# Kernel tuning notes

Measured on AMD Instinct MI355X. Metric: run time of the kernel, lower is better.

Reference implementation:

```python
import jax, jax.numpy as jnp
import numpy as np

B, S, D = 2, 2048, 2048
H = 16
Q_LORA, KV_LORA = 1536, 512
D_NOPE, D_ROPE, D_V = 128, 64, 128
QK_D = D_NOPE + D_ROPE  # 192
EPS = 1e-6
ROPE_THETA = 10000.0


def rms_norm(x, w, eps=EPS):
    return x * jax.lax.rsqrt(jnp.mean(x * x, axis=-1, keepdims=True) + eps) * w


def apply_rope(x, cos, sin):
    # x: [b, s, h, d]; cos/sin: [s, d//2]; pairs are interleaved (x0,x1),(x2,x3),...
    xr, xi = x[..., 0::2], x[..., 1::2]
    c = cos[None, :, None, :]
    s = sin[None, :, None, :]
    yr = xr * c - xi * s
    yi = xr * s + xi * c
    return jnp.stack([yr, yi], axis=-1).reshape(x.shape)


def setup_inputs() -> dict:
    key = jax.random.key(0)
    ks = jax.random.split(key, 8)
    sd = 0.02
    pos = jnp.arange(S, dtype=jnp.float32)
    inv_freq = 1.0 / (ROPE_THETA ** (jnp.arange(0, D_ROPE, 2, dtype=jnp.float32) / D_ROPE))
    ang = pos[:, None] * inv_freq[None, :]  # [S, D_ROPE//2]
    mask = jnp.triu(jnp.full((S, S), float('-inf'), dtype=jnp.float32), k=1)
    return {
        'x': jax.random.normal(ks[0], (B, S, D), dtype=jnp.float32),
        'freqs_cos': jnp.cos(ang),
        'freqs_sin': jnp.sin(ang),
        'mask': mask,
        'wq_a': jax.random.normal(ks[1], (Q_LORA, D), dtype=jnp.float32) * sd,
        'q_norm_w': jnp.ones((Q_LORA,), dtype=jnp.float32),
        'wq_b': jax.random.normal(ks[2], (H * QK_D, Q_LORA), dtype=jnp.float32) * sd,
        'wkv_a': jax.random.normal(ks[3], (KV_LORA + D_ROPE, D), dtype=jnp.float32) * sd,
        'kv_norm_w': jnp.ones((KV_LORA,), dtype=jnp.float32),
        'wkv_b': jax.random.normal(ks[4], (H * (D_NOPE + D_V), KV_LORA), dtype=jnp.float32) * sd,
        'wo': jax.random.normal(ks[5], (D, H * D_V), dtype=jnp.float32) * sd,
    }


def reference(x, freqs_cos, freqs_sin, mask, wq_a, q_norm_w, wq_b, wkv_a, kv_norm_w, wkv_b, wo):
    b, s, _ = x.shape
    # query path: down-proj -> RMSNorm -> up-proj
    q = rms_norm(x @ wq_a.T, q_norm_w) @ wq_b.T          # [b, s, H*QK_D]
    q = q.reshape(b, s, H, QK_D)
    q_nope, q_pe = q[..., :D_NOPE], q[..., D_NOPE:]
    q_pe = apply_rope(q_pe, freqs_cos, freqs_sin)
    # kv path: joint down-proj, split latent / rope key
    kv_full = x @ wkv_a.T                                 # [b, s, KV_LORA + D_ROPE]
    kv, k_pe = kv_full[..., :KV_LORA], kv_full[..., KV_LORA:]
    k_pe = apply_rope(k_pe[:, :, None, :], freqs_cos, freqs_sin)  # [b, s, 1, D_ROPE]
    q = jnp.concatenate([q_nope, q_pe], axis=-1)          # [b, s, H, QK_D]
    kv = rms_norm(kv, kv_norm_w) @ wkv_b.T                # [b, s, H*(D_NOPE+D_V)]
    kv = kv.reshape(b, s, H, D_NOPE + D_V)
    k_nope, v = kv[..., :D_NOPE], kv[..., D_NOPE:]
    k = jnp.concatenate([k_nope, jnp.broadcast_to(k_pe, (b, s, H, D_ROPE))], axis=-1)
    scale = QK_D ** -0.5
    scores = jnp.einsum('bshd,bthd->bsht', q, k) * scale + mask[None, :, None, :]
    probs = jax.nn.softmax(scores.astype(jnp.float32), axis=-1).astype(x.dtype)
    out = jnp.einsum('bsht,bthd->bshd', probs, v).reshape(b, s, H * D_V)
    return out @ wo.T
```

## Files before the change

kernel.cpp:

```cpp
#include <hip/hip_runtime.h>
#include <hip/hip_bf16.h>

typedef __bf16 bf16_t;
typedef __bf16 bf16x8 __attribute__((ext_vector_type(8)));
typedef __bf16 bf16x4 __attribute__((ext_vector_type(4)));
typedef __bf16 bf16x2 __attribute__((ext_vector_type(2)));
typedef float  f32x4  __attribute__((ext_vector_type(4)));
typedef float  f32x16 __attribute__((ext_vector_type(16)));

#define NB 2
#define NS 2048
#define ND 2048
#define NH 16
#define QLORA 1536
#define KVLORA 512
#define DNOPE 128
#define DROPE 64
#define DVDIM 128
#define QKD 192

#define QSCALE 0.10411754f

#if __has_builtin(__builtin_amdgcn_exp2f)
#define EXP2F(x) __builtin_amdgcn_exp2f(x)
#else
#define EXP2F(x) __expf((x) * 0.69314718056f)
#endif
#if __has_builtin(__builtin_amdgcn_rcpf)
#define RCPF(x) __builtin_amdgcn_rcpf(x)
#else
#define RCPF(x) (1.0f / (x))
#endif

typedef __attribute__((address_space(3))) void as3_void;
typedef __attribute__((address_space(1))) const void as1_void;
__device__ __forceinline__ void gload16(const void* g, void* l) {
  __builtin_amdgcn_global_load_lds((as1_void*)g, (as3_void*)l, 16, 0, 0);
}

__device__ __forceinline__ int pack2(float a, float b) {
  bf16x2 t = {(bf16_t)a, (bf16_t)b};
  return __builtin_bit_cast(int, t);
}

__global__ __launch_bounds__(256) void k_cvt_all(
    const float* __restrict__ x, const float* __restrict__ wqa,
    const float* __restrict__ wqb, const float* __restrict__ wkva,
    const float* __restrict__ wkvb, const float* __restrict__ wo,
    bf16_t* __restrict__ xb, bf16_t* __restrict__ wqab, bf16_t* __restrict__ wqbb,
    bf16_t* __restrict__ wkvab, bf16_t* __restrict__ wkvbb, bf16_t* __restrict__ wob) {
  const int c0 = 2097152, c1 = 2883584, c2 = 4063232, c3 = 4358144, c4 = 4882432,
            c5 = 5931008;
  int i = blockIdx.x * 256 + threadIdx.x;
  for (; i < c5; i += gridDim.x * 256) {
    const float* src;
    bf16_t* dst;
    int off;
    if (i < c0) { src = x; dst = xb; off = i; }
    else if (i < c1) { src = wqa; dst = wqab; off = i - c0; }
    else if (i < c2) { src = wqb; dst = wqbb; off = i - c1; }
    else if (i < c3) { src = wkva; dst = wkvab; off = i - c2; }
    else if (i < c4) { src = wkvb; dst = wkvbb; off = i - c3; }
    else { src = wo; dst = wob; off = i - c4; }
    float4 v = reinterpret_cast<const float4*>(src)[off];
    bf16x4 o = {(bf16_t)v.x, (bf16_t)v.y, (bf16_t)v.z, (bf16_t)v.w};
    reinterpret_cast<bf16x4*>(dst)[off] = o;
  }
}

template <int EPI>
__global__ __launch_bounds__(256) void k_gemm_bt(
    const bf16_t* __restrict__ A, const bf16_t* __restrict__ Bw,
    float* __restrict__ Cf, float* __restrict__ Cf2,
    bf16_t* __restrict__ Kout, bf16_t* __restrict__ Vtout,
    const float* __restrict__ fc, const float* __restrict__ fs,
    int M, int N, int K) {
  __shared__ bf16_t As[2][128 * 64];
  __shared__ bf16_t Bs[2][128 * 64];
  const int tid = threadIdx.x;
  const int lane = tid & 63;
  const int wave = tid >> 6;
  const int wm = (wave >> 1) * 64, wn = (wave & 1) * 64;
  const int nxt = (N + 127) >> 7;
  const int per = gridDim.x >> 3;
  const int rank = (blockIdx.x & 7) * per + (blockIdx.x >> 3);
  const int by = rank / nxt, bx = rank - by * nxt;
  const int m0 = by * 128, n0 = bx * 128;
  const int l15 = lane & 15, l4 = lane >> 4;
  const int srow = lane >> 3;
  const int scol = ((lane & 7) ^ srow) * 8;

  const f32x4 Z4 = {0.f, 0.f, 0.f, 0.f};
  f32x4 acc[4][4];
#pragma unroll
  for (int i = 0; i < 4; ++i)
#pragma unroll
    for (int j = 0; j < 4; ++j) acc[i][j] = Z4;

  auto stage = [&](int buf, int k0) {
#pragma unroll
    for (int c = 0; c < 4; ++c) {
      int chunk = c * 4 + wave;
      int row = chunk * 8 + srow;
      gload16(A + (size_t)(m0 + row) * K + k0 + scol, &As[buf][chunk * 512]);
      gload16(Bw + (size_t)(n0 + row) * K + k0 + scol, &Bs[buf][chunk * 512]);
    }
  };

  const int nk = K >> 6;
  stage(0, 0);
  int cur = 0;
#pragma unroll 1
  for (int t = 0; t < nk; ++t) {
    if (t + 1 < nk) {
      stage(cur ^ 1, (t + 1) * 64);
      asm volatile("s_waitcnt vmcnt(8)" ::: "memory");
    } else {
      asm volatile("s_waitcnt vmcnt(0)" ::: "memory");
    }
    __builtin_amdgcn_sched_barrier(0);
    __builtin_amdgcn_s_barrier();
    __builtin_amdgcn_sched_barrier(0);
#pragma unroll
    for (int ks = 0; ks < 2; ++ks) {
      int kc = ks * 4 + l4;
      int pc = (kc ^ (l15 & 7)) * 8;
      bf16x8 af[4], bfr[4];
#pragma unroll
      for (int f = 0; f < 4; ++f) {
        af[f] = *reinterpret_cast<const bf16x8*>(&As[cur][(wm + f * 16 + l15) * 64 + pc]);
        bfr[f] = *reinterpret_cast<const bf16x8*>(&Bs[cur][(wn + f * 16 + l15) * 64 + pc]);
      }
#pragma unroll
      for (int fi = 0; fi < 4; ++fi)
#pragma unroll
        for (int fj = 0; fj < 4; ++fj)
          acc[fi][fj] = __builtin_amdgcn_mfma_f32_16x16x32_bf16(af[fi], bfr[fj], acc[fi][fj], 0, 0, 0);
    }
    __builtin_amdgcn_sched_barrier(0);
    __builtin_amdgcn_s_barrier();
    cur ^= 1;
  }

#pragma unroll
  for (int fi = 0; fi < 4; ++fi) {
#pragma unroll
    for (int fj = 0; fj < 4; ++fj) {
      int col = n0 + wn + fj * 16 + l15;
      int row0 = m0 + wm + fi * 16 + l4 * 4;
      if (EPI == 1) {
        int h = col >> 8, rr = col & 255;
        int b = row0 >> 11, s0 = row0 & 2047;
        if (rr < DNOPE) {
#pragma unroll
          for (int r = 0; r < 4; ++r)
            Kout[(((size_t)(b * NH + h)) * NS + s0 + r) * QKD + rr] =
                (bf16_t)acc[fi][fj][r];
        } else {
          bf16x4 pv4 = {(bf16_t)acc[fi][fj][0], (bf16_t)acc[fi][fj][1],
                        (bf16_t)acc[fi][fj][2], (bf16_t)acc[fi][fj][3]};
          *reinterpret_cast<bf16x4*>(
              &Vtout[(((size_t)(b * NH + h)) * DVDIM + (rr - DNOPE)) * NS + s0]) = pv4;
        }
      } else {
#pragma unroll
        for (int r = 0; r < 4; ++r) {
          int row = row0 + r;
          float v = acc[fi][fj][r];
          if (EPI == 0) {
            Cf[(size_t)row * N + col] = v;
          } else if (EPI == 2) {
            int h = col / 192;
            int d = col - h * 192;
            int b = row >> 11, s = row & 2047;
            float y = v;
            if (d >= DNOPE) {
              float pv = __shfl_xor(v, 1);
              int pp = ((d & ~1) - DNOPE) >> 1;
              float c = fc[s * 32 + pp], si = fs[s * 32 + pp];
              y = (col & 1) ? (pv * si + v * c) : (v * c - pv * si);
            }
            Kout[((size_t)(b * NH + h) * NS + s) * QKD + d] = (bf16_t)(y * QSCALE);
          } else {
            int b = row >> 11;
            (void)b;
            if (col < QLORA) Cf[(size_t)row * QLORA + col] = v;
            else if (col < QLORA + KVLORA + DROPE)
              Cf2[(size_t)row * (KVLORA + DROPE) + (col - QLORA)] = v;
          }
        }
      }
    }
  }
}

__global__ __launch_bounds__(256) void k_norm_post(
    const float* __restrict__ qa, const float* __restrict__ qw,
    bf16_t* __restrict__ qan, const float* __restrict__ kvf,
    const float* __restrict__ kw, const float* __restrict__ fc,
    const float* __restrict__ fs, bf16_t* __restrict__ kvn,
    bf16_t* __restrict__ Kb) {
  int row = blockIdx.x;
  __shared__ float red[4];
  {
    const float* rp = qa + (size_t)row * QLORA;
    float ss = 0.f;
    for (int c = threadIdx.x * 4; c < QLORA; c += 1024) {
      float4 v = *reinterpret_cast<const float4*>(rp + c);
      ss += v.x * v.x + v.y * v.y + v.z * v.z + v.w * v.w;
    }
#pragma unroll
    for (int m = 32; m; m >>= 1) ss += __shfl_xor(ss, m);
    if ((threadIdx.x & 63) == 0) red[threadIdx.x >> 6] = ss;
    __syncthreads();
    float tot = red[0] + red[1] + red[2] + red[3];
    float rs = rsqrtf(tot / (float)QLORA + 1e-6f);
    for (int c = threadIdx.x * 4; c < QLORA; c += 1024) {
      float4 v = *reinterpret_cast<const float4*>(rp + c);
      bf16x4 o = {(bf16_t)(v.x * rs * qw[c]), (bf16_t)(v.y * rs * qw[c + 1]),
                  (bf16_t)(v.z * rs * qw[c + 2]), (bf16_t)(v.w * rs * qw[c + 3])};
      *reinterpret_cast<bf16x4*>(qan + (size_t)row * QLORA + c) = o;
    }
  }
  __syncthreads();
  const float* rp = kvf + (size_t)row * (KVLORA + DROPE);
  float ss = 0.f;
  float4 v = {0.f, 0.f, 0.f, 0.f};
  if (threadIdx.x < 128) {
    v = reinterpret_cast<const float4*>(rp)[threadIdx.x];
    ss = v.x * v.x + v.y * v.y + v.z * v.z + v.w * v.w;
  }
#pragma unroll
  for (int m = 32; m; m >>= 1) ss += __shfl_xor(ss, m);
  if ((threadIdx.x & 63) == 0) red[threadIdx.x >> 6] = ss;
  __syncthreads();
  float tot = red[0] + red[1] + red[2] + red[3];
  float rs = rsqrtf(tot / (float)KVLORA + 1e-6f);
  if (threadIdx.x < 128) {
    int c = threadIdx.x * 4;
    bf16x4 o = {(bf16_t)(v.x * rs * kw[c]), (bf16_t)(v.y * rs * kw[c + 1]),
                (bf16_t)(v.z * rs * kw[c + 2]), (bf16_t)(v.w * rs * kw[c + 3])};
    *reinterpret_cast<bf16x4*>(kvn + (size_t)row * KVLORA + c) = o;
  }
  int b = row >> 11, s = row & 2047;
  if (threadIdx.x < 32) {
    int p = threadIdx.x;
    float x0 = rp[KVLORA + 2 * p], x1 = rp[KVLORA + 2 * p + 1];
    float c = fc[s * 32 + p], si = fs[s * 32 + p];
    float yr = x0 * c - x1 * si, yi = x0 * si + x1 * c;
    bf16_t br = (bf16_t)yr, bi = (bf16_t)yi;
    for (int h = 0; h < NH; ++h) {
      size_t ob = ((size_t)(b * NH + h) * NS + s) * QKD + DNOPE;
      Kb[ob + 2 * p] = br;
      Kb[ob + 2 * p + 1] = bi;
    }
  }
}

__global__ __launch_bounds__(256, 2) void k_attn(const bf16_t* __restrict__ Qb,
                                                 const bf16_t* __restrict__ Kb,
                                                 const bf16_t* __restrict__ Vtb,
                                                 bf16_t* __restrict__ Ao) {
  __shared__ bf16x8 Ks8[2][64 * 24];
  __shared__ bf16x8 Vs8[2][128 * 8];
  const int id = blockIdx.x;
  const int bh = id & 31;
  const int aa = (id >> 5) & 7;
  const int qt = (id >> 8) ? aa : (15 - aa);
  const int b = bh >> 4, h = bh & 15;
  const int tid = threadIdx.x;
  const int lane = tid & 63, wave = tid >> 6;
  const int l31 = lane & 31, hi = lane >> 5;
  const int q0w = qt * 128 + wave * 32;
  const int qg = q0w + l31;
  const int c4 = hi * 4;
  const int ntiles = 2 * qt + 2;
  const size_t bhNS = (size_t)bh * NS;

  const bf16_t* KbB = Kb + bhNS * QKD;
  const bf16_t* VtB = Vtb + (size_t)bh * DVDIM * NS;
  int koff[6], voff[4];
#pragma unroll
  for (int i = 0; i < 6; ++i) {
    int p = tid + i * 256;
    int row = p / 24, pc = p % 24;
    int lc = (pc & ~7) | ((pc ^ row) & 7);
    koff[i] = row * QKD + lc * 8;
  }
#pragma unroll
  for (int i = 0; i < 4; ++i) {
    int p = tid + i * 256;
    int row = p >> 3, pc = p & 7;
    int lc = pc ^ (row & 7);
    voff[i] = row * NS + lc * 8;
  }

  auto stageKV = [&](int buf, int kv0) {
    const bf16_t* ksrc = KbB + kv0 * QKD;
    const bf16_t* vsrc = VtB + kv0;
    bf16x8* kdst = &Ks8[buf][wave * 64];
    bf16x8* vdst = &Vs8[buf][wave * 64];
#pragma unroll
    for (int i = 0; i < 6; ++i) gload16(ksrc + koff[i], kdst + i * 256);
#pragma unroll
    for (int i = 0; i < 4; ++i) gload16(vsrc + voff[i], vdst + i * 256);
  };

  bf16x8 qf[12];
  {
    const bf16_t* qp = Qb + (bhNS + qg) * QKD + hi * 8;
#pragma unroll
    for (int ks = 0; ks < 12; ++ks)
      qf[ks] = *reinterpret_cast<const bf16x8*>(qp + ks * 16);
  }

  f32x16 oacc[4];
#pragma unroll
  for (int d = 0; d < 4; ++d) oacc[d] = {};
  float mrun = -3e38f, lrun = 0.f;

  stageKV(0, 0);
  int cur = 0;

#pragma unroll 1
  for (int kt = 0; kt < ntiles; ++kt) {
    const int kv0 = kt * 64;
    if (kt + 1 < ntiles) {
      stageKV(cur ^ 1, kv0 + 64);
      asm volatile("s_waitcnt vmcnt(10)" ::: "memory");
    } else {
      asm volatile("s_waitcnt vmcnt(0)" ::: "memory");
    }
    __builtin_amdgcn_sched_barrier(0);
    __builtin_amdgcn_s_barrier();
    __builtin_amdgcn_sched_barrier(0);

    if (kv0 <= q0w + 31) {
      f32x16 sacc[2];
      sacc[0] = {};
      sacc[1] = {};
      __builtin_amdgcn_s_setprio(1);
#pragma unroll
      for (int ks = 0; ks < 12; ++ks) {
#pragma unroll
        for (int kh = 0; kh < 2; ++kh) {
          int row = kh * 32 + l31;
          int c = ks * 2 + hi;
          int pc = (c & ~7) | ((c ^ row) & 7);
          sacc[kh] = __builtin_amdgcn_mfma_f32_32x32x16_bf16(Ks8[cur][row * 24 + pc],
                                                             qf[ks], sacc[kh], 0, 0, 0);
        }
      }
      __builtin_amdgcn_s_setprio(0);

      const bool diag = (kv0 + 63 > q0w);
      float mloc = -3e38f;
#pragma unroll
      for (int kh = 0; kh < 2; ++kh)
#pragma unroll
        for (int rg = 0; rg < 16; ++rg) {
          float s = sacc[kh][rg];
          if (diag) {
            int kg = kv0 + kh * 32 + (rg & 3) + 8 * (rg >> 2) + c4;
            if (kg > qg) s = -3e38f;
            sacc[kh][rg] = s;
          }
          mloc = fmaxf(mloc, s);
        }
      mloc = fmaxf(mloc, __shfl_xor(mloc, 32));

      if (!__all(mloc <= mrun)) {
        float mn = fmaxf(mrun, mloc);
        float fac = EXP2F(mrun - mn);
        mrun = mn;
        lrun *= fac;
#pragma unroll
        for (int d = 0; d < 4; ++d)
#pragma unroll
          for (int rg = 0; rg < 16; ++rg) oacc[d][rg] *= fac;
      }

      float rsum = 0.f;
      int W[8][2];
#pragma unroll
      for (int kh = 0; kh < 2; ++kh)
#pragma unroll
        for (int g = 0; g < 4; ++g) {
          float p0 = EXP2F(sacc[kh][4 * g + 0] - mrun);
          float p1 = EXP2F(sacc[kh][4 * g + 1] - mrun);
          float p2 = EXP2F(sacc[kh][4 * g + 2] - mrun);
          float p3 = EXP2F(sacc[kh][4 * g + 3] - mrun);
          rsum += (p0 + p1) + (p2 + p3);
          W[kh * 4 + g][0] = pack2(p0, p1);
          W[kh * 4 + g][1] = pack2(p2, p3);
        }
      rsum += __shfl_xor(rsum, 32);
      lrun += rsum;

      bf16x8 pa[4];
#pragma unroll
      for (int pks = 0; pks < 4; ++pks) {
        int kh = pks >> 1, G0 = (pks & 1) * 2;
        int a0 = W[kh * 4 + G0][0], a1 = W[kh * 4 + G0][1];
        int b0 = W[kh * 4 + G0 + 1][0], b1 = W[kh * 4 + G0 + 1][1];
        int own0 = hi ? b0 : a0, own1 = hi ? b1 : a1;
        int oth0 = hi ? a0 : b0, oth1 = hi ? a1 : b1;
        int rc0 = __shfl_xor(oth0, 32), rc1 = __shfl_xor(oth1, 32);
        int4 wv;
        wv.x = hi ? rc0 : own0;
        wv.y = hi ? rc1 : own1;
        wv.z = hi ? own0 : rc0;
        wv.w = hi ? own1 : rc1;
        pa[pks] = __builtin_bit_cast(bf16x8, wv);
      }

      __builtin_amdgcn_s_setprio(1);
#pragma unroll
      for (int pks = 0; pks < 4; ++pks)
#pragma unroll
        for (int dvt = 0; dvt < 4; ++dvt) {
          int row = dvt * 32 + l31;
          int pc = (pks * 2 + hi) ^ (row & 7);
          oacc[dvt] = __builtin_amdgcn_mfma_f32_32x32x16_bf16(Vs8[cur][row * 8 + pc],
                                                              pa[pks], oacc[dvt], 0, 0, 0);
        }
      __builtin_amdgcn_s_setprio(0);
    }

    __builtin_amdgcn_sched_barrier(0);
    __builtin_amdgcn_s_barrier();
    cur ^= 1;
  }

  float lr = RCPF(lrun);
  bf16_t* base = Ao + ((size_t)(b * NS) + qg) * (NH * DVDIM) + h * DVDIM;
#pragma unroll
  for (int dvt = 0; dvt < 4; ++dvt)
#pragma unroll
    for (int rg4 = 0; rg4 < 4; ++rg4) {
      int dv0 = dvt * 32 + 8 * rg4 + c4;
      bf16x4 o = {(bf16_t)(oacc[dvt][rg4 * 4 + 0] * lr),
                  (bf16_t)(oacc[dvt][rg4 * 4 + 1] * lr),
                  (bf16_t)(oacc[dvt][rg4 * 4 + 2] * lr),
                  (bf16_t)(oacc[dvt][rg4 * 4 + 3] * lr)};
      *reinterpret_cast<bf16x4*>(base + dv0) = o;
    }
}

extern "C" void kernel_launch(void* const* d_in, const int* in_sizes, int n_in,
                              void* d_out, int out_size, void* d_ws, size_t ws_size,
                              hipStream_t stream) {
  (void)in_sizes; (void)n_in; (void)out_size; (void)ws_size;
  const float* x = (const float*)d_in[0];
  const float* fcos = (const float*)d_in[1];
  const float* fsin = (const float*)d_in[2];
  const float* wq_a = (const float*)d_in[4];
  const float* q_norm_w = (const float*)d_in[5];
  const float* wq_b = (const float*)d_in[6];
  const float* wkv_a = (const float*)d_in[7];
  const float* kv_norm_w = (const float*)d_in[8];
  const float* wkv_b = (const float*)d_in[9];
  const float* wo = (const float*)d_in[10];
  float* out = (float*)d_out;

  char* p = (char*)d_ws;
  bf16_t* x_bf = (bf16_t*)(p);
  bf16_t* wqa_bf = (bf16_t*)(p + 16777216);
  bf16_t* wkva_bf = (bf16_t*)(p + 23068672);
  bf16_t* wqb_bf = (bf16_t*)(p + 25427968);
  bf16_t* wkvb_bf = (bf16_t*)(p + 34865152);
  bf16_t* wo_bf = (bf16_t*)(p + 39059456);
  float* qa_f32 = (float*)(p + 47448064);
  bf16_t* Kb = (bf16_t*)(p + 47448064);
  bf16_t* qan_bf = (bf16_t*)(p + 72613888);
  bf16_t* Qb = (bf16_t*)(p + 85196800);
  char* r2 = p + 110362624;
  float* kvf_f32 = (float*)(r2);
  bf16_t* kvn_bf = (bf16_t*)(r2 + 9437184);
  bf16_t* Vtb = (bf16_t*)(r2 + 13631488);
  bf16_t* attn_bf = (bf16_t*)(r2 + 30408704);

  k_cvt_all<<<2048, 256, 0, stream>>>(x, wq_a, wq_b, wkv_a, wkv_b, wo, x_bf, wqa_bf,
                                      wqb_bf, wkva_bf, wkvb_bf, wo_bf);

  k_gemm_bt<3><<<dim3(544), 256, 0, stream>>>(x_bf, wqa_bf, qa_f32, kvf_f32,
                                              nullptr, nullptr, nullptr, nullptr,
                                              NB * NS, QLORA + KVLORA + DROPE, ND);
  k_norm_post<<<NB * NS, 256, 0, stream>>>(qa_f32, q_norm_w, qan_bf, kvf_f32,
                                           kv_norm_w, fcos, fsin, kvn_bf, Kb);
  k_gemm_bt<2><<<dim3(768), 256, 0, stream>>>(qan_bf, wqb_bf, nullptr, nullptr, Qb,
                                              nullptr, fcos, fsin, NB * NS, NH * QKD,
                                              QLORA);
  k_gemm_bt<1><<<dim3(1024), 256, 0, stream>>>(kvn_bf, wkvb_bf, nullptr, nullptr, Kb,
                                               Vtb, nullptr, nullptr, NB * NS,
                                               NH * (DNOPE + DVDIM), KVLORA);
  k_attn<<<dim3(512), 256, 0, stream>>>(Qb, Kb, Vtb, attn_bf);
  k_gemm_bt<0><<<dim3(512), 256, 0, stream>>>(attn_bf, wo_bf, out, nullptr, nullptr,
                                              nullptr, nullptr, nullptr, NB * NS, ND,
                                              NH * DVDIM);
}
```

Measured before the change: 349.2 us.

## Load V fragments directly from global into registers instead of LDS staging

The attention kernel no longer stages V tiles through double-buffered shared memory. Each wave now loads its V MFMA operands straight from global memory into registers at the start of every KV tile, and the wait counts are adjusted to match. The s_setprio hints around the MFMA loops are also removed. This frees LDS and removes the V copies through shared memory, which may raise occupancy. In exchange, each wave issues redundant global loads for V (all four waves fetch the same tile), adds 16 vector registers of V data, and leaves those loads unprefetched and exposed to latency within the iteration.

```diff
diff --git a/kernel.cpp b/kernel.cpp
--- a/kernel.cpp
+++ b/kernel.cpp
@@ -182,8 +182,6 @@
             }
             Kout[((size_t)(b * NH + h) * NS + s) * QKD + d] = (bf16_t)(y * QSCALE);
           } else {
-            int b = row >> 11;
-            (void)b;
             if (col < QLORA) Cf[(size_t)row * QLORA + col] = v;
             else if (col < QLORA + KVLORA + DROPE)
               Cf2[(size_t)row * (KVLORA + DROPE) + (col - QLORA)] = v;
@@ -262,7 +260,6 @@
                                                  const bf16_t* __restrict__ Vtb,
                                                  bf16_t* __restrict__ Ao) {
   __shared__ bf16x8 Ks8[2][64 * 24];
-  __shared__ bf16x8 Vs8[2][128 * 8];
   const int id = blockIdx.x;
   const int bh = id & 31;
   const int aa = (id >> 5) & 7;
@@ -279,7 +276,7 @@
 
   const bf16_t* KbB = Kb + bhNS * QKD;
   const bf16_t* VtB = Vtb + (size_t)bh * DVDIM * NS;
-  int koff[6], voff[4];
+  int koff[6];
 #pragma unroll
   for (int i = 0; i < 6; ++i) {
     int p = tid + i * 256;
@@ -287,23 +284,12 @@
     int lc = (pc & ~7) | ((pc ^ row) & 7);
     koff[i] = row * QKD + lc * 8;
   }
-#pragma unroll
-  for (int i = 0; i < 4; ++i) {
-    int p = tid + i * 256;
-    int row = p >> 3, pc = p & 7;
-    int lc = pc ^ (row & 7);
-    voff[i] = row * NS + lc * 8;
-  }
-
-  auto stageKV = [&](int buf, int kv0) {
+
+  auto stageK = [&](int buf, int kv0) {
     const bf16_t* ksrc = KbB + kv0 * QKD;
-    const bf16_t* vsrc = VtB + kv0;
     bf16x8* kdst = &Ks8[buf][wave * 64];
-    bf16x8* vdst = &Vs8[buf][wave * 64];
 #pragma unroll
     for (int i = 0; i < 6; ++i) gload16(ksrc + koff[i], kdst + i * 256);
-#pragma unroll
-    for (int i = 0; i < 4; ++i) gload16(vsrc + voff[i], vdst + i * 256);
   };
 
   bf16x8 qf[12];
@@ -319,17 +305,27 @@
   for (int d = 0; d < 4; ++d) oacc[d] = {};
   float mrun = -3e38f, lrun = 0.f;
 
-  stageKV(0, 0);
+  stageK(0, 0);
   int cur = 0;
 
 #pragma unroll 1
   for (int kt = 0; kt < ntiles; ++kt) {
     const int kv0 = kt * 64;
+    bf16x8 vfr[4][4];
+    {
+      const bf16_t* vb = VtB + kv0 + (size_t)l31 * NS + hi * 8;
+#pragma unroll
+      for (int dvt = 0; dvt < 4; ++dvt)
+#pragma unroll
+        for (int pks = 0; pks < 4; ++pks)
+          vfr[dvt][pks] = *reinterpret_cast<const bf16x8*>(
+              vb + (size_t)(dvt * 32) * NS + pks * 16);
+    }
     if (kt + 1 < ntiles) {
-      stageKV(cur ^ 1, kv0 + 64);
-      asm volatile("s_waitcnt vmcnt(10)" ::: "memory");
+      stageK(cur ^ 1, kv0 + 64);
+      asm volatile("s_waitcnt vmcnt(22)" ::: "memory");
     } else {
-      asm volatile("s_waitcnt vmcnt(0)" ::: "memory");
+      asm volatile("s_waitcnt vmcnt(16)" ::: "memory");
     }
     __builtin_amdgcn_sched_barrier(0);
     __builtin_amdgcn_s_barrier();
@@ -339,7 +335,6 @@
       f32x16 sacc[2];
       sacc[0] = {};
       sacc[1] = {};
-      __builtin_amdgcn_s_setprio(1);
 #pragma unroll
       for (int ks = 0; ks < 12; ++ks) {
 #pragma unroll
@@ -351,7 +346,6 @@
                                                              qf[ks], sacc[kh], 0, 0, 0);
         }
       }
-      __builtin_amdgcn_s_setprio(0);
 
       const bool diag = (kv0 + 63 > q0w);
       float mloc = -3e38f;
@@ -414,17 +408,12 @@
         pa[pks] = __builtin_bit_cast(bf16x8, wv);
       }
 
-      __builtin_amdgcn_s_setprio(1);
 #pragma unroll
       for (int pks = 0; pks < 4; ++pks)
 #pragma unroll
-        for (int dvt = 0; dvt < 4; ++dvt) {
-          int row = dvt * 32 + l31;
-          int pc = (pks * 2 + hi) ^ (row & 7);
-          oacc[dvt] = __builtin_amdgcn_mfma_f32_32x32x16_bf16(Vs8[cur][row * 8 + pc],
-                                                              pa[pks], oacc[dvt], 0, 0, 0);
-        }
-      __builtin_amdgcn_s_setprio(0);
+        for (int dvt = 0; dvt < 4; ++dvt)
+          oacc[dvt] = __builtin_amdgcn_mfma_f32_32x32x16_bf16(vfr[dvt][pks], pa[pks],
+                                                              oacc[dvt], 0, 0, 0);
     }
 
     __builtin_amdgcn_sched_barrier(0);
```

New measurement: 437.4 us. +25.3%, slower.
